# Kernel optimization log

Measured on AMD Instinct MI355X. Metric: run time of the kernel, lower is better.

The kernel has to match this reference:

```python
import jax, jax.numpy as jnp
import numpy as np

N, F_IN, UNITS, HEADS = 8192, 256, 64, 4
NEG_BIG = -1e10


def setup_inputs() -> dict:
    key = jax.random.key(0)
    k1, k2, k3, k4, k5 = jax.random.split(key, 5)
    X = jax.random.normal(k1, (N, F_IN), dtype=jnp.float32)
    # sparse-ish binary adjacency with self-loops (float mask, as used by the module)
    A = (jax.random.uniform(k2, (N, N)) < 0.004).astype(jnp.float32)
    A = jnp.maximum(A, jnp.eye(N, dtype=jnp.float32))
    W = jax.random.normal(k3, (HEADS, F_IN, UNITS), dtype=jnp.float32) * (1.0 / np.sqrt(F_IN))
    attn_self = jax.random.normal(k4, (HEADS, UNITS), dtype=jnp.float32) * (1.0 / np.sqrt(UNITS))
    attn_neigh = jax.random.normal(k5, (HEADS, UNITS), dtype=jnp.float32) * (1.0 / np.sqrt(UNITS))
    return {"X": X, "A": A, "W": W, "attn_self": attn_self, "attn_neigh": attn_neigh}


def reference(X, A, W, attn_self, attn_neigh):
    # per-head linear projection: [H, N, U]
    feats = jnp.einsum('nf,hfu->hnu', X, W)
    a_self = jnp.einsum('hnu,hu->hn', feats, attn_self)    # [H, N]
    a_neigh = jnp.einsum('hnu,hu->hn', feats, attn_neigh)  # [H, N]
    # additive GAT scores: e_ij = a_self_i + a_neigh_j -> [H, N, N]
    scores = a_self[:, :, None] + a_neigh[:, None, :]
    scores = jax.nn.leaky_relu(scores, negative_slope=0.2)
    scores = scores + NEG_BIG * (1.0 - A)  # additive mask on non-edges
    attn = jax.nn.softmax(scores, axis=-1)
    # dropout is identity at training=False (module default)
    out = jnp.einsum('hnm,hmu->hnu', attn, feats)  # [H, N, U]
    # 'concat' reduction: head-major concat along feature dim -> [N, H*U]
    out = jnp.transpose(out, (1, 0, 2)).reshape(N, HEADS * UNITS)
    return jax.nn.elu(out)
```

## Files before the change

### kernel.cpp

```cpp
#include <hip/hip_runtime.h>

#define NN    8192
#define FIN   256
#define UNITS 64
#define HEADS 4
#define CTOT  256
#define CAP   256

__global__ __launch_bounds__(256) void k_proj(const float* __restrict__ X,
                                              const float* __restrict__ W,
                                              const float* __restrict__ atts,
                                              const float* __restrict__ attn,
                                              float* __restrict__ feats,
                                              float* __restrict__ s_self,
                                              float* __restrict__ s_neigh) {
    __shared__ float Xt[32 * 68];
    __shared__ float Wl[32 * 68];
    __shared__ float reds[64];
    __shared__ float redn[64];
    const int tid = threadIdx.x;
    const int r0  = blockIdx.x * 64;
    const int h   = blockIdx.y;

    const int r  = (tid & 15) * 4;
    const int cl = (tid >> 4) * 4;

    const int srow = tid >> 2;
    const int skq  = (tid & 3) * 8;
    const int wk   = tid >> 3;
    const int wu   = (tid & 7) * 8;

    if (tid < 64) { reds[tid] = 0.f; redn[tid] = 0.f; }

    float acc[4][4];
    #pragma unroll
    for (int a = 0; a < 4; ++a)
        #pragma unroll
        for (int b = 0; b < 4; ++b) acc[a][b] = 0.f;

    for (int k0 = 0; k0 < FIN; k0 += 32) {
        __syncthreads();
        {
            const float4* xp = reinterpret_cast<const float4*>(
                X + (size_t)(r0 + srow) * FIN + k0 + skq);
            const float4 x0 = xp[0], x1 = xp[1];
            const float xs[8] = {x0.x, x0.y, x0.z, x0.w, x1.x, x1.y, x1.z, x1.w};
            #pragma unroll
            for (int m = 0; m < 8; ++m) Xt[(skq + m) * 68 + srow] = xs[m];
        }
        {
            const float4* wp = reinterpret_cast<const float4*>(
                W + (size_t)h * (FIN * UNITS) + (size_t)(k0 + wk) * UNITS + wu);
            const float4 w0 = wp[0], w1 = wp[1];
            const float ws8[8] = {w0.x, w0.y, w0.z, w0.w, w1.x, w1.y, w1.z, w1.w};
            #pragma unroll
            for (int m = 0; m < 8; ++m) Wl[wk * 68 + wu + m] = ws8[m];
        }
        __syncthreads();
        #pragma unroll 8
        for (int k = 0; k < 32; ++k) {
            const float4 a4 = *reinterpret_cast<const float4*>(&Xt[k * 68 + r]);
            const float4 b4 = *reinterpret_cast<const float4*>(&Wl[k * 68 + cl]);
            const float av[4] = {a4.x, a4.y, a4.z, a4.w};
            const float bv[4] = {b4.x, b4.y, b4.z, b4.w};
            #pragma unroll
            for (int ri = 0; ri < 4; ++ri)
                #pragma unroll
                for (int ci = 0; ci < 4; ++ci)
                    acc[ri][ci] += av[ri] * bv[ci];
        }
    }

    float as4[4], an4[4];
    #pragma unroll
    for (int ci = 0; ci < 4; ++ci) {
        as4[ci] = atts[h * UNITS + cl + ci];
        an4[ci] = attn[h * UNITS + cl + ci];
    }
    #pragma unroll
    for (int ri = 0; ri < 4; ++ri) {
        float4 o = make_float4(acc[ri][0], acc[ri][1], acc[ri][2], acc[ri][3]);
        *reinterpret_cast<float4*>(&feats[(size_t)(r0 + r + ri) * CTOT + h * UNITS + cl]) = o;
        const float ps = acc[ri][0] * as4[0] + acc[ri][1] * as4[1]
                       + acc[ri][2] * as4[2] + acc[ri][3] * as4[3];
        const float pn = acc[ri][0] * an4[0] + acc[ri][1] * an4[1]
                       + acc[ri][2] * an4[2] + acc[ri][3] * an4[3];
        atomicAdd(&reds[r + ri], ps);
        atomicAdd(&redn[r + ri], pn);
    }
    __syncthreads();
    if (tid < 64) {
        s_self [((size_t)(r0 + tid) << 2) + h] = reds[tid];
        s_neigh[((size_t)(r0 + tid) << 2) + h] = redn[tid];
    }
}

__global__ __launch_bounds__(256) void k_gat(const float* __restrict__ A,
                                             const float* __restrict__ feats,
                                             const float* __restrict__ s_self,
                                             const float* __restrict__ s_neigh,
                                             float* __restrict__ out) {
    __shared__ int   ej[CAP];
    __shared__ float sc[HEADS][CAP];
    __shared__ int   cnt;
    const int tid = threadIdx.x;
    const int i   = blockIdx.x;
    if (tid == 0) cnt = 0;
    __syncthreads();

    {
        const float4* Arow4 = reinterpret_cast<const float4*>(A + (size_t)i * NN);
        unsigned mask = 0;
        #pragma unroll
        for (int q = 0; q < 8; ++q) {
            const float4 v = Arow4[q * 256 + tid];
            mask |= (v.x != 0.f ? 1u : 0u) << (4 * q);
            mask |= (v.y != 0.f ? 1u : 0u) << (4 * q + 1);
            mask |= (v.z != 0.f ? 1u : 0u) << (4 * q + 2);
            mask |= (v.w != 0.f ? 1u : 0u) << (4 * q + 3);
        }
        const int c = __popc(mask);
        int base = 0;
        if (c) base = atomicAdd(&cnt, c);
        while (mask) {
            const int b = __ffs(mask) - 1;
            mask &= mask - 1;
            if (base < CAP) ej[base] = (b >> 2) * 1024 + tid * 4 + (b & 3);
            ++base;
        }
    }
    __syncthreads();
    const int ne = min(cnt, CAP);

    const int w    = tid >> 6;
    const int lane = tid & 63;
    const float si = s_self[((size_t)i << 2) + w];
    float m = -3.0e38f;
    for (int jj = lane; jj < ne; jj += 64) {
        const int j = ej[jj];
        float e = si + s_neigh[((size_t)j << 2) + w];
        e = (e > 0.f) ? e : 0.2f * e;
        sc[w][jj] = e;
        m = fmaxf(m, e);
    }
    #pragma unroll
    for (int off = 32; off > 0; off >>= 1) m = fmaxf(m, __shfl_xor(m, off, 64));
    float l = 0.f;
    for (int jj = lane; jj < ne; jj += 64) {
        const float p = __expf(sc[w][jj] - m);
        sc[w][jj] = p;
        l += p;
    }
    #pragma unroll
    for (int off = 32; off > 0; off >>= 1) l += __shfl_xor(l, off, 64);
    const float rl = 1.f / l;

    const float* fb = feats + tid;
    float o0 = 0.f, o1 = 0.f, o2 = 0.f, o3 = 0.f;
    int jj = 0;
    for (; jj + 4 <= ne; jj += 4) {
        const int ja = ej[jj], jb = ej[jj + 1], jc = ej[jj + 2], jd = ej[jj + 3];
        const float pa = sc[w][jj],     pb = sc[w][jj + 1];
        const float pc = sc[w][jj + 2], pd = sc[w][jj + 3];
        o0 += pa * fb[(size_t)ja * CTOT];
        o1 += pb * fb[(size_t)jb * CTOT];
        o2 += pc * fb[(size_t)jc * CTOT];
        o3 += pd * fb[(size_t)jd * CTOT];
    }
    for (; jj < ne; ++jj) o0 += sc[w][jj] * fb[(size_t)ej[jj] * CTOT];
    const float o = ((o0 + o1) + (o2 + o3)) * rl;
    const float rr = (o > 0.f) ? o : (__expf(o) - 1.f);
    out[(size_t)i * CTOT + tid] = rr;
}

extern "C" void kernel_launch(void* const* d_in, const int* in_sizes, int n_in,
                              void* d_out, int out_size, void* d_ws, size_t ws_size,
                              hipStream_t stream) {
    const float* X    = (const float*)d_in[0];
    const float* A    = (const float*)d_in[1];
    const float* W    = (const float*)d_in[2];
    const float* atts = (const float*)d_in[3];
    const float* attn = (const float*)d_in[4];

    float* feats   = (float*)d_ws;
    float* s_self  = feats  + (size_t)NN * CTOT;
    float* s_neigh = s_self + (size_t)NN * HEADS;

    k_proj<<<dim3(NN / 64, HEADS), 256, 0, stream>>>(X, W, atts, attn,
                                                     feats, s_self, s_neigh);
    k_gat<<<NN, 256, 0, stream>>>(A, feats, s_self, s_neigh, (float*)d_out);
}
```

Before: 397.1 us.

## Move adjacency scan into projection kernel to overlap with GEMM

The dense adjacency row scan, which builds per-row neighbor lists, moves out of the attention kernel and into extra blocks of the projection launch. Those blocks write the compacted indices and counts to workspace, so the 256 MB adjacency read can run alongside the projection GEMM instead of after it. The attention kernel then only loads the small neighbor list per row. This adds a global round trip for the index lists and needs more workspace.

```diff
diff --git a/kernel.cpp b/kernel.cpp
--- a/kernel.cpp
+++ b/kernel.cpp
@@ -6,25 +6,65 @@
 #define HEADS 4
 #define CTOT  256
 #define CAP   256
-
-__global__ __launch_bounds__(256) void k_proj(const float* __restrict__ X,
-                                              const float* __restrict__ W,
-                                              const float* __restrict__ atts,
-                                              const float* __restrict__ attn,
-                                              float* __restrict__ feats,
-                                              float* __restrict__ s_self,
-                                              float* __restrict__ s_neigh) {
+#define PBLK  512
+
+__global__ __launch_bounds__(256) void k_proj_scan(const float* __restrict__ X,
+                                                   const float* __restrict__ W,
+                                                   const float* __restrict__ atts,
+                                                   const float* __restrict__ attn,
+                                                   const float* __restrict__ A,
+                                                   float* __restrict__ feats,
+                                                   float* __restrict__ s_self,
+                                                   float* __restrict__ s_neigh,
+                                                   int*   __restrict__ ej_g,
+                                                   int*   __restrict__ cnt_g) {
+    const int tid = threadIdx.x;
+    const int bid = blockIdx.x;
+
+    if (bid >= PBLK) {
+        __shared__ int ej[CAP];
+        __shared__ int cnt;
+        const int i = bid - PBLK;
+        if (tid == 0) cnt = 0;
+        __syncthreads();
+        {
+            const float4* Arow4 = reinterpret_cast<const float4*>(A + (size_t)i * NN);
+            unsigned mask = 0;
+            #pragma unroll
+            for (int q = 0; q < 8; ++q) {
+                const float4 v = Arow4[q * 256 + tid];
+                mask |= (v.x != 0.f ? 1u : 0u) << (4 * q);
+                mask |= (v.y != 0.f ? 1u : 0u) << (4 * q + 1);
+                mask |= (v.z != 0.f ? 1u : 0u) << (4 * q + 2);
+                mask |= (v.w != 0.f ? 1u : 0u) << (4 * q + 3);
+            }
+            const int c = __popc(mask);
+            int base = 0;
+            if (c) base = atomicAdd(&cnt, c);
+            while (mask) {
+                const int b = __ffs(mask) - 1;
+                mask &= mask - 1;
+                if (base < CAP) ej[base] = (b >> 2) * 1024 + tid * 4 + (b & 3);
+                ++base;
+            }
+        }
+        __syncthreads();
+        const int ne = min(cnt, CAP);
+        if (tid < ne) ej_g[(size_t)i * CAP + tid] = ej[tid];
+        if (tid == 0) cnt_g[i] = ne;
+        return;
+    }
+
     __shared__ float Xt[32 * 68];
     __shared__ float Wl[32 * 68];
     __shared__ float reds[64];
     __shared__ float redn[64];
-    const int tid = threadIdx.x;
-    const int r0  = blockIdx.x * 64;
-    const int h   = blockIdx.y;
+    const int rt = bid & 127;
+    const int h  = bid >> 7;
+    const int r0 = rt * 64;
 
     const int r  = (tid & 15) * 4;
     const int cl = (tid >> 4) * 4;
-
     const int srow = tid >> 2;
     const int skq  = (tid & 3) * 8;
     const int wk   = tid >> 3;
@@ -95,42 +135,19 @@
     }
 }
 
-__global__ __launch_bounds__(256) void k_gat(const float* __restrict__ A,
+__global__ __launch_bounds__(256) void k_gat(const int*   __restrict__ ej_g,
+                                             const int*   __restrict__ cnt_g,
                                              const float* __restrict__ feats,
                                              const float* __restrict__ s_self,
                                              const float* __restrict__ s_neigh,
                                              float* __restrict__ out) {
     __shared__ int   ej[CAP];
     __shared__ float sc[HEADS][CAP];
-    __shared__ int   cnt;
     const int tid = threadIdx.x;
     const int i   = blockIdx.x;
-    if (tid == 0) cnt = 0;
+    const int ne  = cnt_g[i];
+    if (tid < ne) ej[tid] = ej_g[(size_t)i * CAP + tid];
     __syncthreads();
-
-    {
-        const float4* Arow4 = reinterpret_cast<const float4*>(A + (size_t)i * NN);
-        unsigned mask = 0;
-        #pragma unroll
-        for (int q = 0; q < 8; ++q) {
-            const float4 v = Arow4[q * 256 + tid];
-            mask |= (v.x != 0.f ? 1u : 0u) << (4 * q);
-            mask |= (v.y != 0.f ? 1u : 0u) << (4 * q + 1);
-            mask |= (v.z != 0.f ? 1u : 0u) << (4 * q + 2);
-            mask |= (v.w != 0.f ? 1u : 0u) << (4 * q + 3);
-        }
-        const int c = __popc(mask);
-        int base = 0;
-        if (c) base = atomicAdd(&cnt, c);
-        while (mask) {
-            const int b = __ffs(mask) - 1;
-            mask &= mask - 1;
-            if (base < CAP) ej[base] = (b >> 2) * 1024 + tid * 4 + (b & 3);
-            ++base;
-        }
-    }
-    __syncthreads();
-    const int ne = min(cnt, CAP);
 
     const int w    = tid >> 6;
     const int lane = tid & 63;
@@ -185,8 +202,10 @@
     float* feats   = (float*)d_ws;
     float* s_self  = feats  + (size_t)NN * CTOT;
     float* s_neigh = s_self + (size_t)NN * HEADS;
-
-    k_proj<<<dim3(NN / 64, HEADS), 256, 0, stream>>>(X, W, atts, attn,
-                                                     feats, s_self, s_neigh);
-    k_gat<<<NN, 256, 0, stream>>>(A, feats, s_self, s_neigh, (float*)d_out);
+    int*   cnt_g   = (int*)(s_neigh + (size_t)NN * HEADS);
+    int*   ej_g    = cnt_g + NN;
+
+    k_proj_scan<<<PBLK + NN, 256, 0, stream>>>(X, W, atts, attn, A,
+                                               feats, s_self, s_neigh, ej_g, cnt_g);
+    k_gat<<<NN, 256, 0, stream>>>(ej_g, cnt_g, feats, s_self, s_neigh, (float*)d_out);
 }
```

Result: no change. 393.0 us (median of 2 runs) (-1.0%).
